# Kernel tuning notes

Hardware: AMD Instinct MI355X
Metric: run time of the kernel (lower is better)

Reference implementation:

```python
import jax, jax.numpy as jnp
import numpy as np

NUM_HEADS = 16
NUM_T = 8
L1D = 16  # img_size // patch_size


def _freqs_1d(dim, end, base=10000.0):
    f = 1.0 / (base ** (jnp.arange(0, dim, 2, dtype=jnp.float32) / dim))  # [dim/2]
    ang = jnp.outer(jnp.arange(end, dtype=jnp.float32), f)                # [end, dim/2]
    return jnp.cos(ang), jnp.sin(ang)


def _freqs_2d(dim, h, w, base=10000.0):
    f = 1.0 / (base ** (jnp.arange(0, dim, 4, dtype=jnp.float32)[: dim // 4] / dim))  # [dim/4]
    ax = jnp.outer(jnp.arange(w, dtype=jnp.float32), f)  # [w, dim/4]
    ay = jnp.outer(jnp.arange(h, dtype=jnp.float32), f)  # [h, dim/4]
    # flatten order: position index = y*w + x
    ang_x = jnp.broadcast_to(ax[None, :, :], (h, w, dim // 4)).reshape(h * w, dim // 4)
    ang_y = jnp.broadcast_to(ay[:, None, :], (h, w, dim // 4)).reshape(h * w, dim // 4)
    ang = jnp.concatenate([ang_x, ang_y], axis=-1)  # [h*w, dim/2]
    return jnp.cos(ang), jnp.sin(ang)


def _rope(x, cos, sin):
    # x: [..., P, d]; cos/sin: [P, d/2]; interleaved complex pairs (x0,x1),(x2,x3),...
    xr, xi = x[..., 0::2], x[..., 1::2]
    or_ = xr * cos - xi * sin
    oi = xr * sin + xi * cos
    return jnp.stack([or_, oi], axis=-1).reshape(x.shape)


def setup_inputs() -> dict:
    key = jax.random.key(0)
    ks = jax.random.split(key, 5)
    H = 1024
    return {
        "x": jax.random.normal(ks[0], (2, 2048, H), dtype=jnp.float32),
        "w_qkv": jax.random.normal(ks[1], (3 * H, H), dtype=jnp.float32) * 0.02,
        "b_qkv": jax.random.normal(ks[2], (3 * H,), dtype=jnp.float32) * 0.02,
        "w_out": jax.random.normal(ks[3], (H, H), dtype=jnp.float32) * 0.02,
        "b_out": jax.random.normal(ks[4], (H,), dtype=jnp.float32) * 0.02,
    }


def reference(x, w_qkv, b_qkv, w_out, b_out):
    B, L, H = x.shape
    n, t = NUM_HEADS, NUM_T
    hd = H // n
    Ls = L // t  # spatial tokens per frame (= L1D*L1D)

    # QKV projection; per-head layout [q|k|v] of size 3*hd (matches torch rearrange+chunk)
    qkv = (x @ w_qkv.T + b_qkv).reshape(B, L, n, 3 * hd)
    q, k, v = qkv[..., :hd], qkv[..., hd:2 * hd], qkv[..., 2 * hd:]

    cos_s, sin_s = _freqs_2d(hd, L1D, L1D)  # [Ls, hd/2]
    cos_t, sin_t = _freqs_1d(hd, t)         # [t, hd/2]

    def to_bntl(a):  # (B, L=t*Ls, n, hd) -> (B, n, t, Ls, hd)
        return a.reshape(B, t, Ls, n, hd).transpose(0, 3, 1, 2, 4)

    q = _rope(to_bntl(q), cos_s, sin_s)
    k = _rope(to_bntl(k), cos_s, sin_s)
    # temporal rope: rotate over t axis
    q = _rope(q.transpose(0, 1, 3, 2, 4), cos_t, sin_t).transpose(0, 1, 3, 2, 4)
    k = _rope(k.transpose(0, 1, 3, 2, 4), cos_t, sin_t).transpose(0, 1, 3, 2, 4)
    q = q.reshape(B, n, L, hd)
    k = k.reshape(B, n, L, hd)
    v = v.transpose(0, 2, 1, 3)  # (B, n, L, hd)

    scores = jnp.einsum('bnqd,bnkd->bnqk', q, k) / jnp.sqrt(jnp.asarray(hd, jnp.float32))
    idx = jnp.arange(L)
    neg = jnp.finfo(jnp.float32).min
    causal = jnp.where(idx[None, :] <= idx[:, None], 0.0, neg)  # [L, L]
    attn = jax.nn.softmax((scores + causal).astype(jnp.float32), axis=-1).astype(x.dtype)

    o = jnp.einsum('bnqk,bnkd->bnqd', attn, v).transpose(0, 2, 1, 3).reshape(B, L, H)
    o = o * jax.nn.sigmoid(o)  # swish
    return o @ w_out.T + b_out
```

## Files before the change

### kernel.cpp

```cpp
#include <hip/hip_runtime.h>
#include <math.h>

#define B_SZ 2
#define L_SEQ 2048
#define H_SZ 1024
#define NH 16
#define HD 64
#define QSCALE 0.18033688011112042f

typedef __attribute__((ext_vector_type(8))) short frag_ab;
typedef __attribute__((ext_vector_type(4))) float frag_cd;
typedef __attribute__((ext_vector_type(8))) unsigned short u16x8;
typedef __attribute__((ext_vector_type(4))) unsigned short u16x4;

__device__ __forceinline__ unsigned short f2bf(float f) {
  unsigned int x = __builtin_bit_cast(unsigned int, f);
  x += 0x7fffu + ((x >> 16) & 1u);
  return (unsigned short)(x >> 16);
}
__device__ __forceinline__ float bf2f(unsigned int u) {
  return __builtin_bit_cast(float, u << 16);
}
__device__ __forceinline__ unsigned int cvt_pk_bf16(float lo, float hi) {
  unsigned int r;
  asm("v_cvt_pk_bf16_f32 %0, %1, %2" : "=v"(r) : "v"(lo), "v"(hi));
  return r;
}
__device__ __forceinline__ void gload16(const void* g, void* l) {
  __builtin_amdgcn_global_load_lds((const __attribute__((address_space(1))) void*)g,
                                   (__attribute__((address_space(3))) void*)l, 16, 0, 0);
}

__device__ __forceinline__ void cvt8(const float* __restrict__ in,
                                     unsigned short* __restrict__ out, int i) {
  float4 a = *(const float4*)&in[i];
  float4 b = *(const float4*)&in[i + 4];
  u16x8 o = {f2bf(a.x), f2bf(a.y), f2bf(a.z), f2bf(a.w),
             f2bf(b.x), f2bf(b.y), f2bf(b.z), f2bf(b.w)};
  *(u16x8*)&out[i] = o;
}

__global__ __launch_bounds__(256) void glue_pre_k(
    const float* __restrict__ x, const float* __restrict__ wq, const float* __restrict__ wo,
    unsigned short* __restrict__ xb, unsigned short* __restrict__ wqb,
    unsigned short* __restrict__ wob,
    float* __restrict__ cosb, float* __restrict__ sinb) {
  int bx = blockIdx.x, tid = threadIdx.x;
  if (bx < 256) {
    int idx = bx * 256 + tid;
    int l = idx >> 5, j = idx & 31;
    int ti = l >> 8;
    int s = l & 255;
    float ang_s;
    if (j < 16) ang_s = (float)(s & 15) * powf(10000.f, -(float)j / 16.f);
    else        ang_s = (float)(s >> 4) * powf(10000.f, -(float)(j - 16) / 16.f);
    float ang_t = (float)ti * powf(10000.f, -(float)j / 32.f);
    float a = ang_s + ang_t;
    cosb[idx] = cosf(a);
    sinb[idx] = sinf(a);
  } else if (bx < 2304) {
    cvt8(x, xb, ((bx - 256) * 256 + tid) * 8);
  } else if (bx < 3840) {
    cvt8(wq, wqb, ((bx - 2304) * 256 + tid) * 8);
  } else {
    cvt8(wo, wob, ((bx - 3840) * 256 + tid) * 8);
  }
}

template <int BF16_OUT>
__global__ __launch_bounds__(256) void gemm_mfma_k(
    const unsigned short* __restrict__ A, const unsigned short* __restrict__ W,
    const float* __restrict__ bias, void* __restrict__ Cout, int M, int N, int K) {
  __shared__ unsigned short As[2][128 * 32];
  __shared__ unsigned short Ws[2][128 * 32];
  const frag_cd fzero = {0.f, 0.f, 0.f, 0.f};
  int tid = threadIdx.x;
  int nbx = N >> 7;
  int nwg = gridDim.x;
  int bid = blockIdx.x;
  int qq = nwg >> 3;
  int bidx = (bid & 7) * qq + (bid >> 3);
  int m0 = (bidx / nbx) * 128, n0 = (bidx % nbx) * 128;
  int w = tid >> 6, lane = tid & 63, t = lane & 15, g = lane >> 4;
  int wm = w >> 1, wn = w & 1;
  frag_cd acc[4][4];
#pragma unroll
  for (int mi = 0; mi < 4; ++mi)
#pragma unroll
    for (int ni = 0; ni < 4; ++ni) acc[mi][ni] = fzero;

#define G_ISSUE(k0, bi)                                                        \
  _Pragma("unroll") for (int it = 0; it < 2; ++it) {                           \
    int c = tid + it * 256;                                                    \
    int row = c >> 2, e0 = (c & 3) * 8;                                        \
    gload16(A + (size_t)(m0 + row) * K + (k0) + e0, &As[bi][c * 8]);           \
    gload16(W + (size_t)(n0 + row) * K + (k0) + e0, &Ws[bi][c * 8]);           \
  }

  G_ISSUE(0, 0);
  __syncthreads();
  int kb = 0;
  for (int k0 = 0; k0 < K; k0 += 32, kb ^= 1) {
    if (k0 + 32 < K) { G_ISSUE(k0 + 32, kb ^ 1); }
    frag_ab af[4], wf[4];
#pragma unroll
    for (int mi = 0; mi < 4; ++mi)
      af[mi] = *(const frag_ab*)&As[kb][(wm * 64 + mi * 16 + t) * 32 + 8 * g];
#pragma unroll
    for (int ni = 0; ni < 4; ++ni)
      wf[ni] = *(const frag_ab*)&Ws[kb][(wn * 64 + ni * 16 + t) * 32 + 8 * g];
    __builtin_amdgcn_s_setprio(1);
#pragma unroll
    for (int mi = 0; mi < 4; ++mi)
#pragma unroll
      for (int ni = 0; ni < 4; ++ni)
        acc[mi][ni] = __builtin_amdgcn_mfma_f32_16x16x32_bf16(af[mi], wf[ni], acc[mi][ni], 0, 0, 0);
    __builtin_amdgcn_s_setprio(0);
    __syncthreads();
  }
#pragma unroll
  for (int mi = 0; mi < 4; ++mi)
#pragma unroll
    for (int ni = 0; ni < 4; ++ni) {
      int col = n0 + wn * 64 + ni * 16 + t;
      float bv = bias[col];
#pragma unroll
      for (int r = 0; r < 4; ++r) {
        size_t off = (size_t)(m0 + wm * 64 + mi * 16 + g * 4 + r) * N + col;
        float v = acc[mi][ni][r] + bv;
        if (BF16_OUT) ((unsigned short*)Cout)[off] = f2bf(v);
        else          ((float*)Cout)[off] = v;
      }
    }
}

__global__ __launch_bounds__(256) void glue_mid_k(
    const unsigned short* __restrict__ qkvb,
    const float* __restrict__ cosb, const float* __restrict__ sinb,
    unsigned short* __restrict__ Qb, unsigned short* __restrict__ Kb,
    unsigned short* __restrict__ Vt) {
  __shared__ unsigned short Ts[64][72];
  int bx = blockIdx.x, tid0 = threadIdx.x;
  if (bx < 8192) {
    int tid = bx * 256 + tid0;
    int j = tid & 31;
    int n = (tid >> 5) & 15;
    int l = (tid >> 9) & 2047;
    int b = tid >> 20;
    size_t base = ((size_t)(b * L_SEQ + l)) * 3072 + n * 192;
    float cr = cosb[l * 32 + j], sr = sinb[l * 32 + j];
    size_t ob = ((size_t)((b * NH + n) * L_SEQ + l)) * HD + 2 * j;
    unsigned int qw = *(const unsigned int*)(qkvb + base + 2 * j);
    unsigned int kw = *(const unsigned int*)(qkvb + base + 64 + 2 * j);
    float qx = bf2f(qw & 0xffffu), qy = bf2f(qw >> 16);
    float kx = bf2f(kw & 0xffffu), ky = bf2f(kw >> 16);
    unsigned int qo = (unsigned)f2bf((qx * cr - qy * sr) * QSCALE) |
                      ((unsigned)f2bf((qx * sr + qy * cr) * QSCALE) << 16);
    unsigned int ko = (unsigned)f2bf(kx * cr - ky * sr) | ((unsigned)f2bf(kx * sr + ky * cr) << 16);
    *(unsigned int*)&Qb[ob] = qo;
    *(unsigned int*)&Kb[ob] = ko;
  } else {
    int bx2 = bx - 8192;
    int lt = bx2 & 31, n = (bx2 >> 5) & 15, b = bx2 >> 9;
    int r = tid0 >> 2, c0 = (tid0 & 3) * 16;
    const unsigned short* src = qkvb + (size_t)(b * L_SEQ + lt * 64 + r) * 3072 + n * 192 + 128 + c0;
    u16x8 v0 = *(const u16x8*)src;
    u16x8 v1 = *(const u16x8*)(src + 8);
#pragma unroll
    for (int e = 0; e < 8; ++e) {
      Ts[c0 + e][r] = v0[e];
      Ts[c0 + 8 + e][r] = v1[e];
    }
    __syncthreads();
    int d = tid0 >> 2, l0 = (tid0 & 3) * 16;
    u16x8 a = *(const u16x8*)&Ts[d][l0];
    u16x8 b2 = *(const u16x8*)&Ts[d][l0 + 8];
    unsigned short* dst = Vt + ((size_t)((b * NH + n) * HD + d)) * L_SEQ + lt * 64 + l0;
    *(u16x8*)dst = a;
    *(u16x8*)(dst + 8) = b2;
  }
}

__device__ __forceinline__ void attn_tile(
    const unsigned short* __restrict__ Ksb, const unsigned short* __restrict__ Vsb,
    unsigned short* __restrict__ pw,
    const frag_ab* qf, frag_cd* oacc, float& m_run, float& l_run,
    int qrow, bool diag, int kt, int t, int g) {
  const frag_cd fzero = {0.f, 0.f, 0.f, 0.f};
  frag_cd st[4];
  __builtin_amdgcn_s_setprio(1);
#pragma unroll
  for (int kb = 0; kb < 4; ++kb) {
    frag_ab k0f = *(const frag_ab*)&Ksb[(((kb * 16 + t) * 64) + 8 * g) ^ ((t & 7) << 3)];
    frag_ab k1f = *(const frag_ab*)&Ksb[(((kb * 16 + t) * 64) + 32 + 8 * g) ^ ((t & 7) << 3)];
    st[kb] = __builtin_amdgcn_mfma_f32_16x16x32_bf16(k0f, qf[0], fzero, 0, 0, 0);
    st[kb] = __builtin_amdgcn_mfma_f32_16x16x32_bf16(k1f, qf[1], st[kb], 0, 0, 0);
  }
  __builtin_amdgcn_s_setprio(0);
  float sv[16];
  float mx = -1e30f;
#pragma unroll
  for (int kb = 0; kb < 4; ++kb)
#pragma unroll
    for (int r = 0; r < 4; ++r) {
      float x = st[kb][r];
      if (diag && (kt * 64 + kb * 16 + g * 4 + r) > qrow) x = -1e30f;
      sv[kb * 4 + r] = x;
      mx = fmaxf(mx, x);
    }
  mx = fmaxf(mx, __shfl_xor(mx, 16));
  mx = fmaxf(mx, __shfl_xor(mx, 32));
  if (__any(mx > m_run)) {
    float mnew = fmaxf(m_run, mx);
    float coef = __builtin_amdgcn_exp2f(m_run - mnew);
#pragma unroll
    for (int db = 0; db < 4; ++db) oacc[db] *= coef;
    l_run *= coef;
    m_run = mnew;
  }
  float psum = 0.f;
  unsigned int pk[8];
#pragma unroll
  for (int i = 0; i < 8; ++i) {
    float p0 = __builtin_amdgcn_exp2f(sv[2 * i] - m_run);
    float p1 = __builtin_amdgcn_exp2f(sv[2 * i + 1] - m_run);
    psum += p0 + p1;
    pk[i] = cvt_pk_bf16(p0, p1);
  }
  psum += __shfl_xor(psum, 16);
  psum += __shfl_xor(psum, 32);
  l_run += psum;

#pragma unroll
  for (int kb = 0; kb < 4; ++kb) {
    uint2 pr = {pk[kb * 2], pk[kb * 2 + 1]};
    *(uint2*)&pw[(t * 64 + kb * 16 + g * 4) ^ ((t & 7) << 3)] = pr;
  }
  frag_ab pf0 = *(const frag_ab*)&pw[(t * 64 + 8 * g) ^ ((t & 7) << 3)];
  frag_ab pf1 = *(const frag_ab*)&pw[(t * 64 + 32 + 8 * g) ^ ((t & 7) << 3)];
  __builtin_amdgcn_s_setprio(1);
#pragma unroll
  for (int db = 0; db < 4; ++db) {
    frag_ab v0f = *(const frag_ab*)&Vsb[(((db * 16 + t) * 64) + 8 * g) ^ ((t & 7) << 3)];
    frag_ab v1f = *(const frag_ab*)&Vsb[(((db * 16 + t) * 64) + 32 + 8 * g) ^ ((t & 7) << 3)];
    oacc[db] = __builtin_amdgcn_mfma_f32_16x16x32_bf16(v0f, pf0, oacc[db], 0, 0, 0);
    oacc[db] = __builtin_amdgcn_mfma_f32_16x16x32_bf16(v1f, pf1, oacc[db], 0, 0, 0);
  }
  __builtin_amdgcn_s_setprio(0);
}

__global__ __launch_bounds__(512) void attn_mfma_k(
    const unsigned short* __restrict__ Qg, const unsigned short* __restrict__ Kg,
    const unsigned short* __restrict__ Vt, unsigned short* __restrict__ Og) {
  __shared__ unsigned short Ks[2][64 * 64];
  __shared__ unsigned short Vs[2][64 * 64];
  __shared__ unsigned short Ps[8][16 * 64];
  const frag_cd fzero = {0.f, 0.f, 0.f, 0.f};
  int bx = blockIdx.x;
  int qtA = bx & 15;
  int n = (bx >> 4) & 15;
  int b = bx >> 8;
  int qtB = 31 - qtA;
  int tid = threadIdx.x;
  int w = tid >> 6, lane = tid & 63, t = lane & 15, g = lane >> 4;
  int side = w >> 2;
  int qt = side ? qtA : qtB;
  size_t kvbase = ((size_t)(b * NH + n)) * L_SEQ * HD;
  int qrow = qt * 64 + (w & 3) * 16 + t;

  const unsigned short* qp = Qg + kvbase + (size_t)qrow * HD;
  frag_ab qf[2] = {*(const frag_ab*)(qp + 8 * g), *(const frag_ab*)(qp + 32 + 8 * g)};

  frag_cd oacc[4];
#pragma unroll
  for (int db = 0; db < 4; ++db) oacc[db] = fzero;
  float m_run = -1e30f, l_run = 0.f;

  int srow = tid >> 3, se0 = (tid & 7) * 8;
  int sdst = (srow * 64 + se0) ^ ((srow & 7) << 3);
  u16x8 kreg = *(const u16x8*)(Kg + kvbase + (size_t)srow * HD + se0);
  u16x8 vreg = *(const u16x8*)(Vt + kvbase + (size_t)srow * L_SEQ + se0);
  *(u16x8*)&Ks[0][sdst] = kreg;
  *(u16x8*)&Vs[0][sdst] = vreg;

  for (int kt = 0; kt <= qtB; ++kt) {
    int cur = kt & 1;
    __syncthreads();
    if (kt < qtB) {
      kreg = *(const u16x8*)(Kg + kvbase + (size_t)((kt + 1) * 64 + srow) * HD + se0);
      vreg = *(const u16x8*)(Vt + kvbase + (size_t)srow * L_SEQ + (kt + 1) * 64 + se0);
    }
    if (kt <= qt)
      attn_tile(&Ks[cur][0], &Vs[cur][0], &Ps[w][0], qf, oacc, m_run, l_run, qrow,
                kt == qt, kt, t, g);
    if (kt < qtB) {
      int nxt = cur ^ 1;
      *(u16x8*)&Ks[nxt][sdst] = kreg;
      *(u16x8*)&Vs[nxt][sdst] = vreg;
    }
  }

  size_t ob0 = (size_t)b * L_SEQ * H_SZ + n * 64;
  float inv = 1.f / l_run;
#pragma unroll
  for (int db = 0; db < 4; ++db) {
    u16x4 ov;
#pragma unroll
    for (int r = 0; r < 4; ++r) {
      float o = oacc[db][r] * inv;
      o = o / (1.f + __expf(-o));
      ov[r] = f2bf(o);
    }
    *(u16x4*)&Og[ob0 + (size_t)qrow * H_SZ + db * 16 + g * 4] = ov;
  }
}

extern "C" void kernel_launch(void* const* d_in, const int* in_sizes, int n_in,
                              void* d_out, int out_size, void* d_ws, size_t ws_size,
                              hipStream_t stream) {
  const float* x = (const float*)d_in[0];
  const float* w_qkv = (const float*)d_in[1];
  const float* b_qkv = (const float*)d_in[2];
  const float* w_out = (const float*)d_in[3];
  const float* b_out = (const float*)d_in[4];
  float* out = (float*)d_out;

  float* ws = (float*)d_ws;
  float* cosb = ws;
  float* sinb = cosb + 65536;
  unsigned short* us = (unsigned short*)(sinb + 65536);
  unsigned short* qkvb = us;
  unsigned short* Qb = qkvb + 12582912;
  unsigned short* Kb = Qb + 4194304;
  unsigned short* Vt = Kb + 4194304;
  unsigned short* Og = Vt + 4194304;
  unsigned short* xb = Og + 4194304;
  unsigned short* wqkvb = xb + 4194304;
  unsigned short* woutb = wqkvb + 3145728;

  glue_pre_k<<<4352, 256, 0, stream>>>(x, w_qkv, w_out, xb, wqkvb, woutb, cosb, sinb);

  gemm_mfma_k<1><<<768, 256, 0, stream>>>(xb, wqkvb, b_qkv, qkvb, 4096, 3072, 1024);

  glue_mid_k<<<9216, 256, 0, stream>>>(qkvb, cosb, sinb, Qb, Kb, Vt);

  attn_mfma_k<<<B_SZ * NH * 16, 512, 0, stream>>>(Qb, Kb, Vt, Og);

  gemm_mfma_k<0><<<256, 256, 0, stream>>>(Og, woutb, b_out, out, 4096, 1024, 1024);
}
```

Baseline: 125.7 us.

## Fuse RoPE, Q scaling and V transpose into QKV GEMM epilogue

The QKV GEMM epilogue now applies bias, the rotary embedding (using a lane shuffle to fetch the pair partner) and the Q scale, then writes Q, K and transposed V directly. This removes the separate glue_mid kernel and the bf16 qkv intermediate round trip through memory. The cos/sin tables are interleaved into a float2 table. The cost is scattered 2-byte stores and strided V writes in the epilogue, which may coalesce poorly.

Result: faster. 119.4 us (-5.0%).

```diff
diff --git a/kernel.cpp b/kernel.cpp
--- a/kernel.cpp
+++ b/kernel.cpp
@@ -43,8 +43,7 @@
 __global__ __launch_bounds__(256) void glue_pre_k(
     const float* __restrict__ x, const float* __restrict__ wq, const float* __restrict__ wo,
     unsigned short* __restrict__ xb, unsigned short* __restrict__ wqb,
-    unsigned short* __restrict__ wob,
-    float* __restrict__ cosb, float* __restrict__ sinb) {
+    unsigned short* __restrict__ wob, float2* __restrict__ ctab) {
   int bx = blockIdx.x, tid = threadIdx.x;
   if (bx < 256) {
     int idx = bx * 256 + tid;
@@ -56,8 +55,7 @@
     else        ang_s = (float)(s >> 4) * powf(10000.f, -(float)(j - 16) / 16.f);
     float ang_t = (float)ti * powf(10000.f, -(float)j / 32.f);
     float a = ang_s + ang_t;
-    cosb[idx] = cosf(a);
-    sinb[idx] = sinf(a);
+    ctab[idx] = make_float2(cosf(a), sinf(a));
   } else if (bx < 2304) {
     cvt8(x, xb, ((bx - 256) * 256 + tid) * 8);
   } else if (bx < 3840) {
@@ -67,10 +65,20 @@
   }
 }
 
-template <int BF16_OUT>
-__global__ __launch_bounds__(256) void gemm_mfma_k(
+#define G_ISSUE(k0, bi)                                                        \
+  _Pragma("unroll") for (int it = 0; it < 2; ++it) {                           \
+    int c = tid + it * 256;                                                    \
+    int row = c >> 2, e0 = (c & 3) * 8;                                        \
+    gload16(A + (size_t)(m0 + row) * K + (k0) + e0, &As[bi][c * 8]);           \
+    gload16(W + (size_t)(n0 + row) * K + (k0) + e0, &Ws[bi][c * 8]);           \
+  }
+
+__global__ __launch_bounds__(256) void gemm_qkv_fused_k(
     const unsigned short* __restrict__ A, const unsigned short* __restrict__ W,
-    const float* __restrict__ bias, void* __restrict__ Cout, int M, int N, int K) {
+    const float* __restrict__ bias, const float2* __restrict__ ctab,
+    unsigned short* __restrict__ Qb, unsigned short* __restrict__ Kb,
+    unsigned short* __restrict__ Vt) {
+  const int K = 1024, N = 3072;
   __shared__ unsigned short As[2][128 * 32];
   __shared__ unsigned short Ws[2][128 * 32];
   const frag_cd fzero = {0.f, 0.f, 0.f, 0.f};
@@ -89,14 +97,6 @@
 #pragma unroll
     for (int ni = 0; ni < 4; ++ni) acc[mi][ni] = fzero;
 
-#define G_ISSUE(k0, bi)                                                        \
-  _Pragma("unroll") for (int it = 0; it < 2; ++it) {                           \
-    int c = tid + it * 256;                                                    \
-    int row = c >> 2, e0 = (c & 3) * 8;                                        \
-    gload16(A + (size_t)(m0 + row) * K + (k0) + e0, &As[bi][c * 8]);           \
-    gload16(W + (size_t)(n0 + row) * K + (k0) + e0, &Ws[bi][c * 8]);           \
-  }
-
   G_ISSUE(0, 0);
   __syncthreads();
   int kb = 0;
@@ -118,6 +118,89 @@
     __builtin_amdgcn_s_setprio(0);
     __syncthreads();
   }
+
+#pragma unroll
+  for (int ni = 0; ni < 4; ++ni) {
+    int cb = n0 + wn * 64 + ni * 16;
+    int region = (cb >> 6) % 3;
+    int head = cb / 192;
+    int d = (cb & 63) + t;
+    float bv = bias[cb + t];
+    if (region == 2) {
+#pragma unroll
+      for (int mi = 0; mi < 4; ++mi) {
+        int row0 = m0 + wm * 64 + mi * 16 + g * 4;
+        int bb = row0 >> 11, l0 = row0 & 2047;
+        u16x4 ov;
+#pragma unroll
+        for (int r = 0; r < 4; ++r) ov[r] = f2bf(acc[mi][ni][r] + bv);
+        *(u16x4*)&Vt[((size_t)((bb * NH + head) * HD + d)) * L_SEQ + l0] = ov;
+      }
+    } else {
+      float qs = (region == 0) ? QSCALE : 1.f;
+      float sgn = (t & 1) ? qs : -qs;
+      unsigned short* dst = (region == 0) ? Qb : Kb;
+      int j = d >> 1;
+#pragma unroll
+      for (int mi = 0; mi < 4; ++mi) {
+        int row0 = m0 + wm * 64 + mi * 16 + g * 4;
+        int bb = row0 >> 11, l0 = row0 & 2047;
+        size_t obase = ((size_t)(bb * NH + head) * L_SEQ + l0) * HD + d;
+#pragma unroll
+        for (int r = 0; r < 4; ++r) {
+          float v = acc[mi][ni][r] + bv;
+          float p = __shfl_xor(v, 1);
+          float2 cs = ctab[(l0 + r) * 32 + j];
+          float o = v * (cs.x * qs) + p * (cs.y * sgn);
+          dst[obase + (size_t)r * HD] = f2bf(o);
+        }
+      }
+    }
+  }
+}
+
+__global__ __launch_bounds__(256) void gemm_mfma_k(
+    const unsigned short* __restrict__ A, const unsigned short* __restrict__ W,
+    const float* __restrict__ bias, float* __restrict__ C, int M, int N, int K) {
+  __shared__ unsigned short As[2][128 * 32];
+  __shared__ unsigned short Ws[2][128 * 32];
+  const frag_cd fzero = {0.f, 0.f, 0.f, 0.f};
+  int tid = threadIdx.x;
+  int nbx = N >> 7;
+  int nwg = gridDim.x;
+  int bid = blockIdx.x;
+  int qq = nwg >> 3;
+  int bidx = (bid & 7) * qq + (bid >> 3);
+  int m0 = (bidx / nbx) * 128, n0 = (bidx % nbx) * 128;
+  int w = tid >> 6, lane = tid & 63, t = lane & 15, g = lane >> 4;
+  int wm = w >> 1, wn = w & 1;
+  frag_cd acc[4][4];
+#pragma unroll
+  for (int mi = 0; mi < 4; ++mi)
+#pragma unroll
+    for (int ni = 0; ni < 4; ++ni) acc[mi][ni] = fzero;
+
+  G_ISSUE(0, 0);
+  __syncthreads();
+  int kb = 0;
+  for (int k0 = 0; k0 < K; k0 += 32, kb ^= 1) {
+    if (k0 + 32 < K) { G_ISSUE(k0 + 32, kb ^ 1); }
+    frag_ab af[4], wf[4];
+#pragma unroll
+    for (int mi = 0; mi < 4; ++mi)
+      af[mi] = *(const frag_ab*)&As[kb][(wm * 64 + mi * 16 + t) * 32 + 8 * g];
+#pragma unroll
+    for (int ni = 0; ni < 4; ++ni)
+      wf[ni] = *(const frag_ab*)&Ws[kb][(wn * 64 + ni * 16 + t) * 32 + 8 * g];
+    __builtin_amdgcn_s_setprio(1);
+#pragma unroll
+    for (int mi = 0; mi < 4; ++mi)
+#pragma unroll
+      for (int ni = 0; ni < 4; ++ni)
+        acc[mi][ni] = __builtin_amdgcn_mfma_f32_16x16x32_bf16(af[mi], wf[ni], acc[mi][ni], 0, 0, 0);
+    __builtin_amdgcn_s_setprio(0);
+    __syncthreads();
+  }
 #pragma unroll
   for (int mi = 0; mi < 4; ++mi)
 #pragma unroll
@@ -125,60 +208,9 @@
       int col = n0 + wn * 64 + ni * 16 + t;
       float bv = bias[col];
 #pragma unroll
-      for (int r = 0; r < 4; ++r) {
-        size_t off = (size_t)(m0 + wm * 64 + mi * 16 + g * 4 + r) * N + col;
-        float v = acc[mi][ni][r] + bv;
-        if (BF16_OUT) ((unsigned short*)Cout)[off] = f2bf(v);
-        else          ((float*)Cout)[off] = v;
-      }
-    }
-}
-
-__global__ __launch_bounds__(256) void glue_mid_k(
-    const unsigned short* __restrict__ qkvb,
-    const float* __restrict__ cosb, const float* __restrict__ sinb,
-    unsigned short* __restrict__ Qb, unsigned short* __restrict__ Kb,
-    unsigned short* __restrict__ Vt) {
-  __shared__ unsigned short Ts[64][72];
-  int bx = blockIdx.x, tid0 = threadIdx.x;
-  if (bx < 8192) {
-    int tid = bx * 256 + tid0;
-    int j = tid & 31;
-    int n = (tid >> 5) & 15;
-    int l = (tid >> 9) & 2047;
-    int b = tid >> 20;
-    size_t base = ((size_t)(b * L_SEQ + l)) * 3072 + n * 192;
-    float cr = cosb[l * 32 + j], sr = sinb[l * 32 + j];
-    size_t ob = ((size_t)((b * NH + n) * L_SEQ + l)) * HD + 2 * j;
-    unsigned int qw = *(const unsigned int*)(qkvb + base + 2 * j);
-    unsigned int kw = *(const unsigned int*)(qkvb + base + 64 + 2 * j);
-    float qx = bf2f(qw & 0xffffu), qy = bf2f(qw >> 16);
-    float kx = bf2f(kw & 0xffffu), ky = bf2f(kw >> 16);
-    unsigned int qo = (unsigned)f2bf((qx * cr - qy * sr) * QSCALE) |
-                      ((unsigned)f2bf((qx * sr + qy * cr) * QSCALE) << 16);
-    unsigned int ko = (unsigned)f2bf(kx * cr - ky * sr) | ((unsigned)f2bf(kx * sr + ky * cr) << 16);
-    *(unsigned int*)&Qb[ob] = qo;
-    *(unsigned int*)&Kb[ob] = ko;
-  } else {
-    int bx2 = bx - 8192;
-    int lt = bx2 & 31, n = (bx2 >> 5) & 15, b = bx2 >> 9;
-    int r = tid0 >> 2, c0 = (tid0 & 3) * 16;
-    const unsigned short* src = qkvb + (size_t)(b * L_SEQ + lt * 64 + r) * 3072 + n * 192 + 128 + c0;
-    u16x8 v0 = *(const u16x8*)src;
-    u16x8 v1 = *(const u16x8*)(src + 8);
-#pragma unroll
-    for (int e = 0; e < 8; ++e) {
-      Ts[c0 + e][r] = v0[e];
-      Ts[c0 + 8 + e][r] = v1[e];
-    }
-    __syncthreads();
-    int d = tid0 >> 2, l0 = (tid0 & 3) * 16;
-    u16x8 a = *(const u16x8*)&Ts[d][l0];
-    u16x8 b2 = *(const u16x8*)&Ts[d][l0 + 8];
-    unsigned short* dst = Vt + ((size_t)((b * NH + n) * HD + d)) * L_SEQ + lt * 64 + l0;
-    *(u16x8*)dst = a;
-    *(u16x8*)(dst + 8) = b2;
-  }
+      for (int r = 0; r < 4; ++r)
+        C[(size_t)(m0 + wm * 64 + mi * 16 + g * 4 + r) * N + col] = acc[mi][ni][r] + bv;
+    }
 }
 
 __device__ __forceinline__ void attn_tile(
@@ -326,11 +358,9 @@
   float* out = (float*)d_out;
 
   float* ws = (float*)d_ws;
-  float* cosb = ws;
-  float* sinb = cosb + 65536;
-  unsigned short* us = (unsigned short*)(sinb + 65536);
-  unsigned short* qkvb = us;
-  unsigned short* Qb = qkvb + 12582912;
+  float2* ctab = (float2*)ws;
+  unsigned short* us = (unsigned short*)(ws + 131072);
+  unsigned short* Qb = us;
   unsigned short* Kb = Qb + 4194304;
   unsigned short* Vt = Kb + 4194304;
   unsigned short* Og = Vt + 4194304;
@@ -338,13 +368,11 @@
   unsigned short* wqkvb = xb + 4194304;
   unsigned short* woutb = wqkvb + 3145728;
 
-  glue_pre_k<<<4352, 256, 0, stream>>>(x, w_qkv, w_out, xb, wqkvb, woutb, cosb, sinb);
-
-  gemm_mfma_k<1><<<768, 256, 0, stream>>>(xb, wqkvb, b_qkv, qkvb, 4096, 3072, 1024);
-
-  glue_mid_k<<<9216, 256, 0, stream>>>(qkvb, cosb, sinb, Qb, Kb, Vt);
+  glue_pre_k<<<4352, 256, 0, stream>>>(x, w_qkv, w_out, xb, wqkvb, woutb, ctab);
+
+  gemm_qkv_fused_k<<<768, 256, 0, stream>>>(xb, wqkvb, b_qkv, ctab, Qb, Kb, Vt);
 
   attn_mfma_k<<<B_SZ * NH * 16, 512, 0, stream>>>(Qb, Kb, Vt, Og);
 
-  gemm_mfma_k<0><<<256, 256, 0, stream>>>(Og, woutb, b_out, out, 4096, 1024, 1024);
-}
+  gemm_mfma_k<<<256, 256, 0, stream>>>(Og, woutb, b_out, out, 4096, 1024, 1024);
+}
```
